# Kernel tuning notes

Measured on AMD Instinct MI355X. Metric: run time of the kernel, lower is better.

## Reference

```python
import jax, jax.numpy as jnp
import numpy as np

N, D, E = 50000, 128, 600000
EPS = 1e-5  # LayerNorm eps (torch default)


def setup_inputs() -> dict:
    key = jax.random.key(0)
    ks = jax.random.split(key, 8)
    s = D ** -0.5
    return {
        "in_feat": jax.random.normal(ks[0], (N, D), dtype=jnp.float32),
        "edge_src": jax.random.randint(ks[1], (E,), 0, N),
        "edge_dst": jax.random.randint(ks[2], (E,), 0, N),
        "W1": jax.random.normal(ks[3], (D, D), dtype=jnp.float32) * s,
        "b1": jnp.zeros((D,), jnp.float32),
        "W2": jax.random.normal(ks[4], (D, D), dtype=jnp.float32) * s,
        "b2": jnp.zeros((D,), jnp.float32),
        "ln1_w": jnp.ones((D,), jnp.float32),
        "ln1_b": jnp.zeros((D,), jnp.float32),
        "ln2_w": jnp.ones((D,), jnp.float32),
        "ln2_b": jnp.zeros((D,), jnp.float32),
    }


def layer_norm(x, w, b):
    mu = jnp.mean(x, axis=-1, keepdims=True)
    var = jnp.var(x, axis=-1, keepdims=True)
    return (x - mu) * jax.lax.rsqrt(var + EPS) * w + b


def gcn_conv(x, W, b, src, dst, deg_inv_sqrt):
    # PyG GCNConv: linear transform, then D^-1/2 (A+I) D^-1/2 propagation, then bias
    h = x @ W  # [N, D]
    norm = deg_inv_sqrt[src] * deg_inv_sqrt[dst]  # [E]
    agg = jax.ops.segment_sum(h[src] * norm[:, None], dst, num_segments=N)
    agg = agg + (deg_inv_sqrt ** 2)[:, None] * h  # self-loop term handled analytically
    return agg + b


def reference(in_feat, W1, b1, W2, b2, ln1_w, ln1_b, ln2_w, ln2_b, edge_src, edge_dst):
    # degree with self-loops, computed on destination (PyG convention)
    deg = jax.ops.segment_sum(jnp.ones((E,), in_feat.dtype), edge_dst, num_segments=N) + 1.0
    dis = jax.lax.rsqrt(deg)
    h = gcn_conv(in_feat, W1, b1, edge_src, edge_dst, dis)
    ori = in_feat  # in_feats == h_feats -> residual uses original input
    ln_params = [(ln1_w, ln1_b), (ln2_w, ln2_b)]
    for i in range(2):  # prop_step - 1 iterations
        h = h + ori  # res=True, residual=1.0
        h = layer_norm(h, *ln_params[i])
        h = jax.nn.relu(h)  # dropout=0 -> identity
        h = gcn_conv(h, W2, b2, edge_src, edge_dst, dis)
    return h
```

## Files before the change

### kernel.cpp

```cpp
#include <hip/hip_runtime.h>
#include <hip/hip_bf16.h>

typedef unsigned short bf16_t;
typedef __attribute__((ext_vector_type(4))) float f32x4;
typedef __attribute__((ext_vector_type(8))) unsigned short us8;

#define CAP 64

__device__ __forceinline__ float bf2f(bf16_t u) {
  return __uint_as_float(((unsigned int)u) << 16);
}
__device__ __forceinline__ bf16_t f2bf(float f) {
  unsigned int u = __float_as_uint(f);
  return (bf16_t)((u + 0x7FFFu + ((u >> 16) & 1u)) >> 16);
}
__device__ __forceinline__ void acc2(float2& a, unsigned int d) {
  a.x += __uint_as_float(d << 16);
  a.y += __uint_as_float(d & 0xffff0000u);
}

__global__ void UnifiedGNN_56521769616171_kernel() {}


__global__ void gnn_zero(int* cnt, int n, bf16_t* Azrow,
                         const float* W1, const float* W2,
                         bf16_t* Wt1g, bf16_t* Wt2g,
                         int4* csr4, long ncsr4, int nzero) {
  long gid = (long)blockIdx.x * 256 + threadIdx.x;
  long stride = (long)gridDim.x * 256;
  if (blockIdx.x == 0 && threadIdx.x < 64)
    ((unsigned int*)Azrow)[threadIdx.x] = 0u;
  if (gid < 4096) {
    const float* W = (gid < 2048) ? W1 : W2;
    bf16_t* dst = (gid < 2048) ? Wt1g : Wt2g;
    int j = (int)(gid & 2047);
    int c = j & 127;
    int kb = j >> 7;
    int k0 = kb << 3;
    us8 v;
#pragma unroll
    for (int q = 0; q < 8; q++) v[q] = f2bf(W[(size_t)(k0 + q) * 128 + c]);
    ((us8*)dst)[c * 16 + (kb ^ (c & 15))] = v;
  }
  for (long i = gid; i < n; i += stride) cnt[i] = 0;
  int4 nv = make_int4(nzero, nzero, nzero, nzero);
  for (long i = gid; i < ncsr4; i += stride) csr4[i] = nv;
}

__global__ void gnn_fill(const int* src, const int* dst, int* cnt,
                         int* csr, int e, int n) {
  int i = blockIdx.x * 256 + threadIdx.x;
  if (i < e) {
    int d = dst[i];
    if (d >= 0 && d < n) {
      int pos = atomicAdd(&cnt[d], 1);
      if (pos < CAP) csr[(size_t)d * CAP + pos] = src[i];
    }
  }
}

__global__ __launch_bounds__(512) void gnn_gemm(const void* Xv,
    const bf16_t* Wg, const int* cnt, bf16_t* A, int n, int xfmt) {
  __shared__ __align__(16) bf16_t Wt[128 * 128];
  int tid = threadIdx.x;

  for (int j = tid; j < 2048; j += 512)
    ((us8*)Wt)[j] = ((const us8*)Wg)[j];
  __syncthreads();

  int lane = tid & 63;
  int wid = tid >> 6;
  int l15 = lane & 15;
  int lk = lane >> 4;
  const bf16_t* Xb = (const bf16_t*)Xv;
  const float* Xf = (const float*)Xv;

  int rowbase = blockIdx.x * 128 + wid * 16;
  int arow = rowbase + l15;
  int arc = arow < n ? arow : (n - 1);

  f32x4 acc[8];
#pragma unroll
  for (int c = 0; c < 8; c++) {
    acc[c][0] = 0.0f; acc[c][1] = 0.0f; acc[c][2] = 0.0f; acc[c][3] = 0.0f;
  }

#pragma unroll
  for (int ks = 0; ks < 4; ks++) {
    int kb = ks * 4 + lk;
    us8 ah, al;
    if (xfmt == 0) {
      float4 a0 = *(const float4*)(Xf + (size_t)arc * 128 + kb * 8);
      float4 a1 = *(const float4*)(Xf + (size_t)arc * 128 + kb * 8 + 4);
      ah[0] = f2bf(a0.x); al[0] = f2bf(a0.x - bf2f(ah[0]));
      ah[1] = f2bf(a0.y); al[1] = f2bf(a0.y - bf2f(ah[1]));
      ah[2] = f2bf(a0.z); al[2] = f2bf(a0.z - bf2f(ah[2]));
      ah[3] = f2bf(a0.w); al[3] = f2bf(a0.w - bf2f(ah[3]));
      ah[4] = f2bf(a1.x); al[4] = f2bf(a1.x - bf2f(ah[4]));
      ah[5] = f2bf(a1.y); al[5] = f2bf(a1.y - bf2f(ah[5]));
      ah[6] = f2bf(a1.z); al[6] = f2bf(a1.z - bf2f(ah[6]));
      ah[7] = f2bf(a1.w); al[7] = f2bf(a1.w - bf2f(ah[7]));
    } else {
      ah = *(const us8*)(Xb + (size_t)arc * 128 + kb * 8);
    }
#pragma unroll
    for (int c = 0; c < 8; c++) {
      int col = c * 16 + l15;
      us8 bf = *(const us8*)&Wt[col * 128 + ((kb ^ l15) << 3)];
      asm volatile("s_nop 2\n\tv_mfma_f32_16x16x32_bf16 %0, %1, %2, %0"
                   : "+v"(acc[c]) : "v"(ah), "v"(bf));
    }
    if (xfmt == 0) {
#pragma unroll
      for (int c = 0; c < 8; c++) {
        int col = c * 16 + l15;
        us8 bf = *(const us8*)&Wt[col * 128 + ((kb ^ l15) << 3)];
        asm volatile("s_nop 2\n\tv_mfma_f32_16x16x32_bf16 %0, %1, %2, %0"
                     : "+v"(acc[c]) : "v"(al), "v"(bf));
      }
    }
  }
  asm volatile("s_nop 7\n\ts_nop 7"
               : "+v"(acc[0]), "+v"(acc[1]), "+v"(acc[2]), "+v"(acc[3]),
                 "+v"(acc[4]), "+v"(acc[5]), "+v"(acc[6]), "+v"(acc[7]));

#pragma unroll
  for (int j = 0; j < 4; j++) {
    int row = rowbase + lk * 4 + j;
    if (row < n) {
      float dd = rsqrtf((float)cnt[row] + 1.0f);
#pragma unroll
      for (int c = 0; c < 8; c++) {
        A[(size_t)row * 128 + c * 16 + l15] = f2bf(acc[c][j] * dd);
      }
    }
  }
}

__global__ void gnn_aggln(const bf16_t* A,
    const int* cnt, const int* csr, const float* bias,
    const float* ori, const float* lnw, const float* lnb,
    bf16_t* Bout, float* Fout, int n, int do_ln) {
  int wid = threadIdx.x >> 6;
  int lane = threadIdx.x & 63;
  int g = lane >> 4;
  int l16 = lane & 15;
  int row = blockIdx.x * 16 + wid * 4 + g;
  bool active = row < n;
  int rc = active ? row : (n - 1);
  int c = cnt[rc];
  int pc = (c + 15) & ~15;
  if (pc > CAP) pc = CAP;
  const int* crow = csr + (size_t)rc * CAP;
  const uint4* Av4 = (const uint4*)A;

  float2 ac[4];
#pragma unroll
  for (int i = 0; i < 4; i++) ac[i] = make_float2(0.0f, 0.0f);

  for (int e = 0; e < pc; e += 16) {
    int sv = crow[e + l16];
#pragma unroll
    for (int half = 0; half < 2; half++) {
      uint4 va[8];
#pragma unroll
      for (int j = 0; j < 8; j++) {
        int s = __shfl(sv, (g << 4) + half * 8 + j);
        va[j] = Av4[(size_t)s * 16 + l16];
      }
#pragma unroll
      for (int j = 0; j < 8; j++) {
        acc2(ac[0], va[j].x);
        acc2(ac[1], va[j].y);
        acc2(ac[2], va[j].z);
        acc2(ac[3], va[j].w);
      }
    }
  }
  {
    uint4 sv4 = Av4[(size_t)rc * 16 + l16];
    acc2(ac[0], sv4.x);
    acc2(ac[1], sv4.y);
    acc2(ac[2], sv4.z);
    acc2(ac[3], sv4.w);
  }

  float dd = rsqrtf((float)c + 1.0f);
  float4 bb0 = *(const float4*)(bias + l16 * 8);
  float4 bb1 = *(const float4*)(bias + l16 * 8 + 4);
  float h[8];
  h[0] = dd * ac[0].x + bb0.x; h[1] = dd * ac[0].y + bb0.y;
  h[2] = dd * ac[1].x + bb0.z; h[3] = dd * ac[1].y + bb0.w;
  h[4] = dd * ac[2].x + bb1.x; h[5] = dd * ac[2].y + bb1.y;
  h[6] = dd * ac[3].x + bb1.z; h[7] = dd * ac[3].y + bb1.w;

  if (do_ln) {
    float4 o0 = *(const float4*)(ori + (size_t)rc * 128 + l16 * 8);
    float4 o1 = *(const float4*)(ori + (size_t)rc * 128 + l16 * 8 + 4);
    float v[8];
    v[0] = h[0] + o0.x; v[1] = h[1] + o0.y; v[2] = h[2] + o0.z; v[3] = h[3] + o0.w;
    v[4] = h[4] + o1.x; v[5] = h[5] + o1.y; v[6] = h[6] + o1.z; v[7] = h[7] + o1.w;
    float s = 0.0f, sq = 0.0f;
#pragma unroll
    for (int i = 0; i < 8; i++) { s += v[i]; sq += v[i] * v[i]; }
    for (int off = 8; off >= 1; off >>= 1) {
      s += __shfl_xor(s, off);
      sq += __shfl_xor(sq, off);
    }
    float mu = s * (1.0f / 128.0f);
    float var = sq * (1.0f / 128.0f) - mu * mu;
    float inv = rsqrtf(var + 1e-5f);
    float4 w0 = *(const float4*)(lnw + l16 * 8);
    float4 w1 = *(const float4*)(lnw + l16 * 8 + 4);
    float4 c0 = *(const float4*)(lnb + l16 * 8);
    float4 c1 = *(const float4*)(lnb + l16 * 8 + 4);
    float wv[8] = {w0.x, w0.y, w0.z, w0.w, w1.x, w1.y, w1.z, w1.w};
    float cv[8] = {c0.x, c0.y, c0.z, c0.w, c1.x, c1.y, c1.z, c1.w};
    us8 o8;
#pragma unroll
    for (int i = 0; i < 8; i++) {
      float y = (v[i] - mu) * inv * wv[i] + cv[i];
      if (y < 0.0f) y = 0.0f;
      o8[i] = f2bf(y);
    }
    if (active) *(us8*)(Bout + (size_t)rc * 128 + l16 * 8) = o8;
  } else {
    if (active) {
      float4 f0 = make_float4(h[0], h[1], h[2], h[3]);
      float4 f1 = make_float4(h[4], h[5], h[6], h[7]);
      *(float4*)(Fout + (size_t)rc * 128 + l16 * 8) = f0;
      *(float4*)(Fout + (size_t)rc * 128 + l16 * 8 + 4) = f1;
    }
  }
}


extern "C" void kernel_launch(void* const* d_in, const int* in_sizes, int n_in,
                              void* d_out, int out_size, void* d_ws, size_t ws_size,
                              hipStream_t stream) {
  UnifiedGNN_56521769616171_kernel<<<1, 64, 0, stream>>>();

  int nI = (n_in > 0 && n_in <= 16) ? n_in : 11;
  long best = -1;
  int iFeat = 0;
  for (int i = 0; i < nI; i++)
    if ((long)in_sizes[i] > best) { best = in_sizes[i]; iFeat = i; }
  int iW[2], iV[6], iE[2];
  int nW = 0, nV = 0, nE = 0;
  for (int i = 0; i < nI; i++) {
    if (i == iFeat) continue;
    int s = in_sizes[i];
    if (s == 128 * 128) { if (nW < 2) iW[nW++] = i; }
    else if (s == 128)  { if (nV < 6) iV[nV++] = i; }
    else                { if (nE < 2) iE[nE++] = i; }
  }
  int aFeat = 0, aEs = 1, aEd = 2, aW1 = 3, aB1 = 4, aW2 = 5, aB2 = 6,
      aL1w = 7, aL1b = 8, aL2w = 9, aL2b = 10;
  if (nW == 2 && nV == 6 && nE == 2) {
    aFeat = iFeat;
    aEs = iE[0]; aEd = iE[1];
    aW1 = iW[0]; aW2 = iW[1];
    aB1 = iV[0]; aB2 = iV[1];
    aL1w = iV[2]; aL1b = iV[3]; aL2w = iV[4]; aL2b = iV[5];
  }

  int N = 50000;
  int E = 600000;
  if (in_sizes[aFeat] > 0 && (in_sizes[aFeat] % 128) == 0) N = in_sizes[aFeat] / 128;
  if (in_sizes[aEs] > 0) E = in_sizes[aEs];

  const float* in_feat = (const float*)d_in[aFeat];
  const int*   esrc    = (const int*)d_in[aEs];
  const int*   edst    = (const int*)d_in[aEd];
  const float* W1      = (const float*)d_in[aW1];
  const float* b1      = (const float*)d_in[aB1];
  const float* W2      = (const float*)d_in[aW2];
  const float* b2      = (const float*)d_in[aB2];
  const float* ln1w    = (const float*)d_in[aL1w];
  const float* ln1b    = (const float*)d_in[aL1b];
  const float* ln2w    = (const float*)d_in[aL2w];
  const float* ln2b    = (const float*)d_in[aL2b];

  char* base = (char*)d_ws;
  size_t off = 0;
  int* cnt = (int*)(base + off);      off += ((size_t)N * 4 + 255) & ~(size_t)255;
  int* csr = (int*)(base + off);      off += ((size_t)N * CAP * 4 + 255) & ~(size_t)255;
  bf16_t* A = (bf16_t*)(base + off);  off += ((size_t)(N + 1) * 256 + 255) & ~(size_t)255;
  bf16_t* B = (bf16_t*)(base + off);  off += ((size_t)N * 256 + 255) & ~(size_t)255;
  bf16_t* Wt1g = (bf16_t*)(base + off); off += 32768;
  bf16_t* Wt2g = (bf16_t*)(base + off); off += 32768;

  long ncsr4 = (long)N * (CAP / 4);
  int gE = (E + 255) / 256;
  int nt128 = (N + 127) / 128;
  int agg_grid = (N + 15) / 16;

  gnn_zero<<<2048, 256, 0, stream>>>(cnt, N, A + (size_t)N * 128, W1, W2,
                                     Wt1g, Wt2g, (int4*)csr, ncsr4, N);
  gnn_fill<<<gE, 256, 0, stream>>>(esrc, edst, cnt, csr, E, N);

  gnn_gemm<<<nt128, 512, 0, stream>>>(in_feat, Wt1g, cnt, A, N, 0);
  gnn_aggln<<<agg_grid, 256, 0, stream>>>(A, cnt, csr, b1, in_feat,
                                          ln1w, ln1b, B, (float*)nullptr, N, 1);

  gnn_gemm<<<nt128, 512, 0, stream>>>(B, Wt2g, cnt, A, N, 1);
  gnn_aggln<<<agg_grid, 256, 0, stream>>>(A, cnt, csr, b2, in_feat,
                                          ln2w, ln2b, B, (float*)nullptr, N, 1);

  gnn_gemm<<<nt128, 512, 0, stream>>>(B, Wt2g, cnt, A, N, 1);
  gnn_aggln<<<agg_grid, 256, 0, stream>>>(A, cnt, csr, b2,
                                          (const float*)nullptr, (const float*)nullptr,
                                          (const float*)nullptr, (bf16_t*)nullptr,
                                          (float*)d_out, N, 0);
}
```

Measured before the change: 246.3 us.

## Skip CSR padding prefill; mask padded neighbor slots in aggregation instead

The zero kernel no longer writes the sentinel index into the whole N×64 CSR buffer, which was a large memory write. Instead the aggregation kernel replaces slots past each row's count with the zero-row index n at read time. The fill kernel now handles two edges per thread with int2 loads and uses nontemporal stores for the CSR writes. In exchange the aggregation loop gains a per-lane compare, and the zero kernel launch shrinks to cover only the counts.

```diff
diff --git a/kernel.cpp b/kernel.cpp
--- a/kernel.cpp
+++ b/kernel.cpp
@@ -24,16 +24,14 @@
 
 __global__ void gnn_zero(int* cnt, int n, bf16_t* Azrow,
                          const float* W1, const float* W2,
-                         bf16_t* Wt1g, bf16_t* Wt2g,
-                         int4* csr4, long ncsr4, int nzero) {
-  long gid = (long)blockIdx.x * 256 + threadIdx.x;
-  long stride = (long)gridDim.x * 256;
+                         bf16_t* Wt1g, bf16_t* Wt2g) {
+  int gid = blockIdx.x * 256 + threadIdx.x;
   if (blockIdx.x == 0 && threadIdx.x < 64)
     ((unsigned int*)Azrow)[threadIdx.x] = 0u;
   if (gid < 4096) {
     const float* W = (gid < 2048) ? W1 : W2;
     bf16_t* dst = (gid < 2048) ? Wt1g : Wt2g;
-    int j = (int)(gid & 2047);
+    int j = gid & 2047;
     int c = j & 127;
     int kb = j >> 7;
     int k0 = kb << 3;
@@ -42,19 +40,32 @@
     for (int q = 0; q < 8; q++) v[q] = f2bf(W[(size_t)(k0 + q) * 128 + c]);
     ((us8*)dst)[c * 16 + (kb ^ (c & 15))] = v;
   }
-  for (long i = gid; i < n; i += stride) cnt[i] = 0;
-  int4 nv = make_int4(nzero, nzero, nzero, nzero);
-  for (long i = gid; i < ncsr4; i += stride) csr4[i] = nv;
+  if (gid < n) cnt[gid] = 0;
 }
 
 __global__ void gnn_fill(const int* src, const int* dst, int* cnt,
                          int* csr, int e, int n) {
   int i = blockIdx.x * 256 + threadIdx.x;
-  if (i < e) {
-    int d = dst[i];
+  int i0 = i * 2;
+  if (i0 + 1 < e) {
+    int2 d2 = *(const int2*)(dst + i0);
+    int2 s2 = *(const int2*)(src + i0);
+    if (d2.x >= 0 && d2.x < n) {
+      int pos = atomicAdd(&cnt[d2.x], 1);
+      if (pos < CAP)
+        __builtin_nontemporal_store(s2.x, &csr[(size_t)d2.x * CAP + pos]);
+    }
+    if (d2.y >= 0 && d2.y < n) {
+      int pos = atomicAdd(&cnt[d2.y], 1);
+      if (pos < CAP)
+        __builtin_nontemporal_store(s2.y, &csr[(size_t)d2.y * CAP + pos]);
+    }
+  } else if (i0 < e) {
+    int d = dst[i0];
     if (d >= 0 && d < n) {
       int pos = atomicAdd(&cnt[d], 1);
-      if (pos < CAP) csr[(size_t)d * CAP + pos] = src[i];
+      if (pos < CAP)
+        __builtin_nontemporal_store(src[i0], &csr[(size_t)d * CAP + pos]);
     }
   }
 }
@@ -159,7 +170,8 @@
   for (int i = 0; i < 4; i++) ac[i] = make_float2(0.0f, 0.0f);
 
   for (int e = 0; e < pc; e += 16) {
-    int sv = crow[e + l16];
+    int raw = crow[e + l16];
+    int sv = (e + l16 < c) ? raw : n;
 #pragma unroll
     for (int half = 0; half < 2; half++) {
       uint4 va[8];
@@ -290,14 +302,14 @@
   bf16_t* Wt1g = (bf16_t*)(base + off); off += 32768;
   bf16_t* Wt2g = (bf16_t*)(base + off); off += 32768;
 
-  long ncsr4 = (long)N * (CAP / 4);
-  int gE = (E + 255) / 256;
+  int gZ = (N + 255) / 256;
+  int gE2 = ((E + 1) / 2 + 255) / 256;
   int nt128 = (N + 127) / 128;
   int agg_grid = (N + 15) / 16;
 
-  gnn_zero<<<2048, 256, 0, stream>>>(cnt, N, A + (size_t)N * 128, W1, W2,
-                                     Wt1g, Wt2g, (int4*)csr, ncsr4, N);
-  gnn_fill<<<gE, 256, 0, stream>>>(esrc, edst, cnt, csr, E, N);
+  gnn_zero<<<gZ, 256, 0, stream>>>(cnt, N, A + (size_t)N * 128, W1, W2,
+                                   Wt1g, Wt2g);
+  gnn_fill<<<gE2, 256, 0, stream>>>(esrc, edst, cnt, csr, E, N);
 
   gnn_gemm<<<nt128, 512, 0, stream>>>(in_feat, Wt1g, cnt, A, N, 0);
   gnn_aggln<<<agg_grid, 256, 0, stream>>>(A, cnt, csr, b1, in_feat,
```

New measurement: 261.4 us. 6.1% more time.

## Fuse aggregation+LayerNorm with next GEMM and drop CSR padding prefill

Applied to the files above, without the earlier changes.

Adds a kernel that aggregates neighbours, applies residual+LayerNorm+ReLU into a swizzled LDS tile, then runs the MFMA GEMM on that tile, replacing two aggregate/GEMM kernel pairs. This removes the global write and re-read of the intermediate bf16 B buffer and two launches. The full CSR fill with a sentinel is replaced by masking padded slots to the zero row at read time, which needs a second zero-padded A buffer for ping-pong. Each fused block now does both the irregular gather and the GEMM with 64KB of LDS, which may lower occupancy and latency hiding for the gather phase.

```diff
diff --git a/kernel.cpp b/kernel.cpp
--- a/kernel.cpp
+++ b/kernel.cpp
@@ -22,18 +22,18 @@
 __global__ void UnifiedGNN_56521769616171_kernel() {}
 
 
-__global__ void gnn_zero(int* cnt, int n, bf16_t* Azrow,
+__global__ void gnn_zero(int* cnt, int n, bf16_t* Azrow, bf16_t* A2zrow,
                          const float* W1, const float* W2,
-                         bf16_t* Wt1g, bf16_t* Wt2g,
-                         int4* csr4, long ncsr4, int nzero) {
-  long gid = (long)blockIdx.x * 256 + threadIdx.x;
-  long stride = (long)gridDim.x * 256;
-  if (blockIdx.x == 0 && threadIdx.x < 64)
+                         bf16_t* Wt1g, bf16_t* Wt2g) {
+  int gid = blockIdx.x * 256 + threadIdx.x;
+  if (blockIdx.x == 0 && threadIdx.x < 64) {
     ((unsigned int*)Azrow)[threadIdx.x] = 0u;
+    ((unsigned int*)A2zrow)[threadIdx.x] = 0u;
+  }
   if (gid < 4096) {
     const float* W = (gid < 2048) ? W1 : W2;
     bf16_t* dst = (gid < 2048) ? Wt1g : Wt2g;
-    int j = (int)(gid & 2047);
+    int j = gid & 2047;
     int c = j & 127;
     int kb = j >> 7;
     int k0 = kb << 3;
@@ -42,9 +42,7 @@
     for (int q = 0; q < 8; q++) v[q] = f2bf(W[(size_t)(k0 + q) * 128 + c]);
     ((us8*)dst)[c * 16 + (kb ^ (c & 15))] = v;
   }
-  for (long i = gid; i < n; i += stride) cnt[i] = 0;
-  int4 nv = make_int4(nzero, nzero, nzero, nzero);
-  for (long i = gid; i < ncsr4; i += stride) csr4[i] = nv;
+  if (gid < n) cnt[gid] = 0;
 }
 
 __global__ void gnn_fill(const int* src, const int* dst, int* cnt,
@@ -137,10 +135,145 @@
   }
 }
 
+__global__ __launch_bounds__(512) void gnn_agg_gemm(const bf16_t* Ain,
+    const int* cnt, const int* csr, const float* bias, const float* ori,
+    const float* lnw, const float* lnb, const bf16_t* Wg,
+    bf16_t* Aout, int n) {
+  __shared__ __align__(16) bf16_t Wt[128 * 128];
+  __shared__ __align__(16) bf16_t Bs[128 * 128];
+  int tid = threadIdx.x;
+  int lane = tid & 63;
+  int wid = tid >> 6;
+  int g = lane >> 4;
+  int l16 = lane & 15;
+
+  for (int j = tid; j < 2048; j += 512)
+    ((us8*)Wt)[j] = ((const us8*)Wg)[j];
+
+  const uint4* Av4 = (const uint4*)Ain;
+
+  for (int rr = 0; rr < 4; rr++) {
+    int rt = wid * 16 + rr * 4 + g;
+    int row = blockIdx.x * 128 + rt;
+    int rc = row < n ? row : (n - 1);
+    int c = cnt[rc];
+    int pc = (c + 15) & ~15;
+    if (pc > CAP) pc = CAP;
+    const int* crow = csr + (size_t)rc * CAP;
+
+    float2 ac[4];
+#pragma unroll
+    for (int i = 0; i < 4; i++) ac[i] = make_float2(0.0f, 0.0f);
+
+    for (int e = 0; e < pc; e += 16) {
+      int raw = crow[e + l16];
+      int sv = (e + l16 < c) ? raw : n;
+#pragma unroll
+      for (int half = 0; half < 2; half++) {
+        uint4 va[8];
+#pragma unroll
+        for (int j = 0; j < 8; j++) {
+          int s = __shfl(sv, (g << 4) + half * 8 + j);
+          va[j] = Av4[(size_t)s * 16 + l16];
+        }
+#pragma unroll
+        for (int j = 0; j < 8; j++) {
+          acc2(ac[0], va[j].x);
+          acc2(ac[1], va[j].y);
+          acc2(ac[2], va[j].z);
+          acc2(ac[3], va[j].w);
+        }
+      }
+    }
+    {
+      uint4 sv4 = Av4[(size_t)rc * 16 + l16];
+      acc2(ac[0], sv4.x);
+      acc2(ac[1], sv4.y);
+      acc2(ac[2], sv4.z);
+      acc2(ac[3], sv4.w);
+    }
+
+    float dd = rsqrtf((float)c + 1.0f);
+    float4 bb0 = *(const float4*)(bias + l16 * 8);
+    float4 bb1 = *(const float4*)(bias + l16 * 8 + 4);
+    float4 o0 = *(const float4*)(ori + (size_t)rc * 128 + l16 * 8);
+    float4 o1 = *(const float4*)(ori + (size_t)rc * 128 + l16 * 8 + 4);
+    float v[8];
+    v[0] = dd * ac[0].x + bb0.x + o0.x; v[1] = dd * ac[0].y + bb0.y + o0.y;
+    v[2] = dd * ac[1].x + bb0.z + o0.z; v[3] = dd * ac[1].y + bb0.w + o0.w;
+    v[4] = dd * ac[2].x + bb1.x + o1.x; v[5] = dd * ac[2].y + bb1.y + o1.y;
+    v[6] = dd * ac[3].x + bb1.z + o1.z; v[7] = dd * ac[3].y + bb1.w + o1.w;
+    float s = 0.0f, sq = 0.0f;
+#pragma unroll
+    for (int i = 0; i < 8; i++) { s += v[i]; sq += v[i] * v[i]; }
+    for (int off = 8; off >= 1; off >>= 1) {
+      s += __shfl_xor(s, off);
+      sq += __shfl_xor(sq, off);
+    }
+    float mu = s * (1.0f / 128.0f);
+    float var = sq * (1.0f / 128.0f) - mu * mu;
+    float inv = rsqrtf(var + 1e-5f);
+    float4 w0 = *(const float4*)(lnw + l16 * 8);
+    float4 w1 = *(const float4*)(lnw + l16 * 8 + 4);
+    float4 c0 = *(const float4*)(lnb + l16 * 8);
+    float4 c1 = *(const float4*)(lnb + l16 * 8 + 4);
+    float wv[8] = {w0.x, w0.y, w0.z, w0.w, w1.x, w1.y, w1.z, w1.w};
+    float cv[8] = {c0.x, c0.y, c0.z, c0.w, c1.x, c1.y, c1.z, c1.w};
+    us8 o8;
+#pragma unroll
+    for (int i = 0; i < 8; i++) {
+      float y = (v[i] - mu) * inv * wv[i] + cv[i];
+      if (y < 0.0f) y = 0.0f;
+      o8[i] = f2bf(y);
+    }
+    *(us8*)&Bs[rt * 128 + ((l16 ^ (rt & 15)) << 3)] = o8;
+  }
+
+  __syncthreads();
+
+  int l15 = lane & 15;
+  int lk = lane >> 4;
+  int rowbase = blockIdx.x * 128 + wid * 16;
+  int rt0 = wid * 16 + l15;
+
+  f32x4 acc[8];
+#pragma unroll
+  for (int c = 0; c < 8; c++) {
+    acc[c][0] = 0.0f; acc[c][1] = 0.0f; acc[c][2] = 0.0f; acc[c][3] = 0.0f;
+  }
+
+#pragma unroll
+  for (int ks = 0; ks < 4; ks++) {
+    int kb = ks * 4 + lk;
+    us8 ah = *(const us8*)&Bs[rt0 * 128 + ((kb ^ l15) << 3)];
+#pragma unroll
+    for (int c = 0; c < 8; c++) {
+      int col = c * 16 + l15;
+      us8 bf = *(const us8*)&Wt[col * 128 + ((kb ^ l15) << 3)];
+      asm volatile("s_nop 2\n\tv_mfma_f32_16x16x32_bf16 %0, %1, %2, %0"
+                   : "+v"(acc[c]) : "v"(ah), "v"(bf));
+    }
+  }
+  asm volatile("s_nop 7\n\ts_nop 7"
+               : "+v"(acc[0]), "+v"(acc[1]), "+v"(acc[2]), "+v"(acc[3]),
+                 "+v"(acc[4]), "+v"(acc[5]), "+v"(acc[6]), "+v"(acc[7]));
+
+#pragma unroll
+  for (int j = 0; j < 4; j++) {
+    int row = rowbase + lk * 4 + j;
+    if (row < n) {
+      float dd = rsqrtf((float)cnt[row] + 1.0f);
+#pragma unroll
+      for (int c = 0; c < 8; c++) {
+        Aout[(size_t)row * 128 + c * 16 + l15] = f2bf(acc[c][j] * dd);
+      }
+    }
+  }
+}
+
 __global__ void gnn_aggln(const bf16_t* A,
     const int* cnt, const int* csr, const float* bias,
-    const float* ori, const float* lnw, const float* lnb,
-    bf16_t* Bout, float* Fout, int n, int do_ln) {
+    float* Fout, int n) {
   int wid = threadIdx.x >> 6;
   int lane = threadIdx.x & 63;
   int g = lane >> 4;
@@ -159,7 +292,8 @@
   for (int i = 0; i < 4; i++) ac[i] = make_float2(0.0f, 0.0f);
 
   for (int e = 0; e < pc; e += 16) {
-    int sv = crow[e + l16];
+    int raw = crow[e + l16];
+    int sv = (e + l16 < c) ? raw : n;
 #pragma unroll
     for (int half = 0; half < 2; half++) {
       uint4 va[8];
@@ -188,49 +322,13 @@
   float dd = rsqrtf((float)c + 1.0f);
   float4 bb0 = *(const float4*)(bias + l16 * 8);
   float4 bb1 = *(const float4*)(bias + l16 * 8 + 4);
-  float h[8];
-  h[0] = dd * ac[0].x + bb0.x; h[1] = dd * ac[0].y + bb0.y;
-  h[2] = dd * ac[1].x + bb0.z; h[3] = dd * ac[1].y + bb0.w;
-  h[4] = dd * ac[2].x + bb1.x; h[5] = dd * ac[2].y + bb1.y;
-  h[6] = dd * ac[3].x + bb1.z; h[7] = dd * ac[3].y + bb1.w;
-
-  if (do_ln) {
-    float4 o0 = *(const float4*)(ori + (size_t)rc * 128 + l16 * 8);
-    float4 o1 = *(const float4*)(ori + (size_t)rc * 128 + l16 * 8 + 4);
-    float v[8];
-    v[0] = h[0] + o0.x; v[1] = h[1] + o0.y; v[2] = h[2] + o0.z; v[3] = h[3] + o0.w;
-    v[4] = h[4] + o1.x; v[5] = h[5] + o1.y; v[6] = h[6] + o1.z; v[7] = h[7] + o1.w;
-    float s = 0.0f, sq = 0.0f;
-#pragma unroll
-    for (int i = 0; i < 8; i++) { s += v[i]; sq += v[i] * v[i]; }
-    for (int off = 8; off >= 1; off >>= 1) {
-      s += __shfl_xor(s, off);
-      sq += __shfl_xor(sq, off);
-    }
-    float mu = s * (1.0f / 128.0f);
-    float var = sq * (1.0f / 128.0f) - mu * mu;
-    float inv = rsqrtf(var + 1e-5f);
-    float4 w0 = *(const float4*)(lnw + l16 * 8);
-    float4 w1 = *(const float4*)(lnw + l16 * 8 + 4);
-    float4 c0 = *(const float4*)(lnb + l16 * 8);
-    float4 c1 = *(const float4*)(lnb + l16 * 8 + 4);
-    float wv[8] = {w0.x, w0.y, w0.z, w0.w, w1.x, w1.y, w1.z, w1.w};
-    float cv[8] = {c0.x, c0.y, c0.z, c0.w, c1.x, c1.y, c1.z, c1.w};
-    us8 o8;
-#pragma unroll
-    for (int i = 0; i < 8; i++) {
-      float y = (v[i] - mu) * inv * wv[i] + cv[i];
-      if (y < 0.0f) y = 0.0f;
-      o8[i] = f2bf(y);
-    }
-    if (active) *(us8*)(Bout + (size_t)rc * 128 + l16 * 8) = o8;
-  } else {
-    if (active) {
-      float4 f0 = make_float4(h[0], h[1], h[2], h[3]);
-      float4 f1 = make_float4(h[4], h[5], h[6], h[7]);
-      *(float4*)(Fout + (size_t)rc * 128 + l16 * 8) = f0;
-      *(float4*)(Fout + (size_t)rc * 128 + l16 * 8 + 4) = f1;
-    }
+  if (active) {
+    float4 f0 = make_float4(dd * ac[0].x + bb0.x, dd * ac[0].y + bb0.y,
+                            dd * ac[1].x + bb0.z, dd * ac[1].y + bb0.w);
+    float4 f1 = make_float4(dd * ac[2].x + bb1.x, dd * ac[2].y + bb1.y,
+                            dd * ac[3].x + bb1.z, dd * ac[3].y + bb1.w);
+    *(float4*)(Fout + (size_t)rc * 128 + l16 * 8) = f0;
+    *(float4*)(Fout + (size_t)rc * 128 + l16 * 8 + 4) = f1;
   }
 }
 
@@ -286,30 +384,26 @@
   int* cnt = (int*)(base + off);      off += ((size_t)N * 4 + 255) & ~(size_t)255;
   int* csr = (int*)(base + off);      off += ((size_t)N * CAP * 4 + 255) & ~(size_t)255;
   bf16_t* A = (bf16_t*)(base + off);  off += ((size_t)(N + 1) * 256 + 255) & ~(size_t)255;
-  bf16_t* B = (bf16_t*)(base + off);  off += ((size_t)N * 256 + 255) & ~(size_t)255;
+  bf16_t* A2 = (bf16_t*)(base + off); off += ((size_t)(N + 1) * 256 + 255) & ~(size_t)255;
   bf16_t* Wt1g = (bf16_t*)(base + off); off += 32768;
   bf16_t* Wt2g = (bf16_t*)(base + off); off += 32768;
 
-  long ncsr4 = (long)N * (CAP / 4);
+  int gZ = (N + 255) / 256;
   int gE = (E + 255) / 256;
   int nt128 = (N + 127) / 128;
   int agg_grid = (N + 15) / 16;
 
-  gnn_zero<<<2048, 256, 0, stream>>>(cnt, N, A + (size_t)N * 128, W1, W2,
-                                     Wt1g, Wt2g, (int4*)csr, ncsr4, N);
+  gnn_zero<<<gZ, 256, 0, stream>>>(cnt, N, A + (size_t)N * 128,
+                                   A2 + (size_t)N * 128, W1, W2, Wt1g, Wt2g);
   gnn_fill<<<gE, 256, 0, stream>>>(esrc, edst, cnt, csr, E, N);
 
   gnn_gemm<<<nt128, 512, 0, stream>>>(in_feat, Wt1g, cnt, A, N, 0);
-  gnn_aggln<<<agg_grid, 256, 0, stream>>>(A, cnt, csr, b1, in_feat,
-                                          ln1w, ln1b, B, (float*)nullptr, N, 1);
-
-  gnn_gemm<<<nt128, 512, 0, stream>>>(B, Wt2g, cnt, A, N, 1);
-  gnn_aggln<<<agg_grid, 256, 0, stream>>>(A, cnt, csr, b2, in_feat,
-                                          ln2w, ln2b, B, (float*)nullptr, N, 1);
-
-  gnn_gemm<<<nt128, 512, 0, stream>>>(B, Wt2g, cnt, A, N, 1);
-  gnn_aggln<<<agg_grid, 256, 0, stream>>>(A, cnt, csr, b2,
-                                          (const float*)nullptr, (const float*)nullptr,
-                                          (const float*)nullptr, (bf16_t*)nullptr,
-                                          (float*)d_out, N, 0);
-}
+
+  gnn_agg_gemm<<<nt128, 512, 0, stream>>>(A, cnt, csr, b1, in_feat,
+                                          ln1w, ln1b, Wt2g, A2, N);
+
+  gnn_agg_gemm<<<nt128, 512, 0, stream>>>(A2, cnt, csr, b2, in_feat,
+                                          ln2w, ln2b, Wt2g, A, N);
+
+  gnn_aggln<<<agg_grid, 256, 0, stream>>>(A, cnt, csr, b2, (float*)d_out, N);
+}
```

New measurement: 248.4 us. No clear change (+0.8%).
